# Performance work log

Measured on AMD Instinct MI355X. Metric: run time of the kernel, lower is better.

## Reference

```python
import jax, jax.numpy as jnp
import numpy as np

B, N, E = 8, 1024, 512
H, D = 8, 64
F = 2048


def setup_inputs() -> dict:
    key = jax.random.key(0)
    ks = jax.random.split(key, 12)
    s = lambda *sh: 1.0 / np.sqrt(sh[-1])
    inp = {
        "input1": jax.random.normal(ks[0], (B, N, E), dtype=jnp.float32),
        # projection weights stored as [in, out] (torch weight transposed)
        "Wq": jax.random.normal(ks[1], (E, H * D), dtype=jnp.float32) * s(E, E),
        "Wk": jax.random.normal(ks[2], (E, H * D), dtype=jnp.float32) * s(E, E),
        "Wv": jax.random.normal(ks[3], (E, H * D), dtype=jnp.float32) * s(E, E),
        "Wo": jax.random.normal(ks[4], (H * D, E), dtype=jnp.float32) * s(E, E),
        "bo": jnp.zeros((E,), dtype=jnp.float32),
        "g1": jnp.ones((E,), dtype=jnp.float32),
        "b1": jnp.zeros((E,), dtype=jnp.float32),
        "W1": jax.random.normal(ks[5], (E, F), dtype=jnp.float32) * s(E, E),
        "bf1": jnp.zeros((F,), dtype=jnp.float32),
        "W2": jax.random.normal(ks[6], (F, E), dtype=jnp.float32) * s(F, F),
        "bf2": jnp.zeros((E,), dtype=jnp.float32),
        "g2": jnp.ones((E,), dtype=jnp.float32),
        "b2": jnp.zeros((E,), dtype=jnp.float32),
    }
    return inp


def _layernorm(x, g, b, eps=1e-5):
    mu = jnp.mean(x, axis=-1, keepdims=True)
    var = jnp.var(x, axis=-1, keepdims=True)
    return (x - mu) * jax.lax.rsqrt(var + eps) * g + b


def reference(input1, Wq, Wk, Wv, Wo, bo, g1, b1, W1, bf1, W2, bf2, g2, b2):
    x = input1
    # QKV projections, split heads: [B, H, N, D]
    q = (x @ Wq).reshape(B, N, H, D).transpose(0, 2, 1, 3)
    k = (x @ Wk).reshape(B, N, H, D).transpose(0, 2, 1, 3)
    v = (x @ Wv).reshape(B, N, H, D).transpose(0, 2, 1, 3)
    # scaled dot-product attention (naive, materialized scores as in source)
    score = jnp.einsum("bhnd,bhmd->bhnm", q, k) / jnp.sqrt(jnp.float32(D))
    weights = jax.nn.softmax(score, axis=-1)
    out = jnp.einsum("bhnm,bhmd->bhnd", weights, v)
    out_concat = out.transpose(0, 2, 1, 3).reshape(B, N, H * D)
    mh = out_concat @ Wo + bo
    out1 = _layernorm(x + mh, g1, b1)
    ff = jax.nn.relu(out1 @ W1 + bf1) @ W2 + bf2
    out3 = _layernorm(out1 + ff, g2, b2)
    return (out3, 0)
```

## Files before the change

kernel.cpp:

```cpp
#include <hip/hip_runtime.h>
#include <cstdint>
#include <cstddef>

typedef _Float16 h8 __attribute__((ext_vector_type(8)));
typedef _Float16 h4 __attribute__((ext_vector_type(4)));
typedef __fp16   g2 __attribute__((ext_vector_type(2)));
typedef float    f32x4 __attribute__((ext_vector_type(4)));

constexpr int B_ = 8, N_ = 1024, E_ = 512, H_ = 8, D_ = 64, F_ = 2048;
constexpr int M_ = B_ * N_;
constexpr int HD_ = H_ * D_;

#define QSCALE2 0.18033688011112042f

#define GLOAD_LDS16(gp, lp)                                                        \
    __builtin_amdgcn_global_load_lds((const __attribute__((address_space(1))) void*)(gp), \
                                     (__attribute__((address_space(3))) void*)(lp), 16, 0, 0)

__device__ __forceinline__ float exp2_raw(float x) {
#if __has_builtin(__builtin_amdgcn_exp2f)
    return __builtin_amdgcn_exp2f(x);
#else
    float r;
    asm("v_exp_f32 %0, %1\n\ts_nop 0" : "=v"(r) : "v"(x));
    return r;
#endif
}

__global__ void __launch_bounds__(256) k_pre(
    const float* __restrict__ x, _Float16* __restrict__ xh,
    const float* __restrict__ Wq, const float* __restrict__ Wk,
    const float* __restrict__ Wv, const float* __restrict__ Wo,
    const float* __restrict__ W1, const float* __restrict__ W2,
    _Float16* __restrict__ oqkv, _Float16* __restrict__ oo,
    _Float16* __restrict__ o1, _Float16* __restrict__ o2) {
    if (blockIdx.z == 12) {
        int i = (blockIdx.x * 256 + threadIdx.x) * 16;
#pragma unroll
        for (int j = 0; j < 4; ++j) {
            float4 v = *(const float4*)(x + i + j * 4);
            h4 o = {(_Float16)v.x, (_Float16)v.y, (_Float16)v.z, (_Float16)v.w};
            *(h4*)(xh + i + j * 4) = o;
        }
        return;
    }
    if (blockIdx.x >= 256) return;
    const float* in;
    _Float16* out;
    int R, C, gt = blockIdx.x;
    switch (blockIdx.z) {
        case 0: in = Wq; out = oqkv;              R = 512;  C = 512;  break;
        case 1: in = Wk; out = oqkv + 512 * 512;  R = 512;  C = 512;  break;
        case 2: in = Wv; out = oqkv + 1024 * 512; R = 512;  C = 512;  break;
        case 3: in = Wo; out = oo;                R = 512;  C = 512;  break;
        default:
            if (blockIdx.z < 8) { in = W1; out = o1; R = 512;  C = 2048; gt += (blockIdx.z - 4) * 256; }
            else                { in = W2; out = o2; R = 2048; C = 512;  gt += (blockIdx.z - 8) * 256; }
    }
    const int ctiles = C >> 5;
    const int ty = gt / ctiles, tx = gt - ty * ctiles;
    const int r0 = ty * 32, c0 = tx * 32;
    __shared__ float lt[32][33];
    const int rr = threadIdx.x >> 3, cq = threadIdx.x & 7;
    float4 v = *(const float4*)&in[(size_t)(r0 + rr) * C + c0 + cq * 4];
    lt[rr][cq * 4 + 0] = v.x; lt[rr][cq * 4 + 1] = v.y;
    lt[rr][cq * 4 + 2] = v.z; lt[rr][cq * 4 + 3] = v.w;
    __syncthreads();
    h4 o = {(_Float16)lt[cq * 4 + 0][rr], (_Float16)lt[cq * 4 + 1][rr],
            (_Float16)lt[cq * 4 + 2][rr], (_Float16)lt[cq * 4 + 3][rr]};
    *(h4*)&out[(size_t)(c0 + rr) * R + r0 + cq * 4] = o;
}

template <int EPI>
__global__ void __launch_bounds__(256) k_gemm(
    const _Float16* __restrict__ A, const _Float16* __restrict__ Bt,
    int Mg, int Ng, int Kg,
    const float* __restrict__ bias,
    _Float16* __restrict__ outh,
    _Float16* __restrict__ qp, _Float16* __restrict__ kp, _Float16* __restrict__ vtp) {
    constexpr int BN = 128;
    constexpr int WN = BN / 2;
    constexpr int NI = WN / 16;
    constexpr int NT = 8;
    __shared__ alignas(16) _Float16 lA[3][64 * 64];
    __shared__ alignas(16) _Float16 lB[3][BN * 64];

    const int tid = threadIdx.x;
    const int lane = tid & 63;
    const int wid = tid >> 6;
    const int wr = wid >> 1, wc = wid & 1;
    const int r16 = lane & 15, hseg = lane >> 4;

    const int bid = blockIdx.x;
    const int xcd = bid & 7;
    const int rem = bid >> 3;
    const int tx = rem >> 4, tyl = rem & 15;
    const int m0 = (xcd * 16 + tyl) * 64;
    const int n0 = tx * BN;

    auto STAGE = [&](int buf, int k0) {
#pragma unroll
        for (int i = 0; i < 2; ++i) {
            const int slot = i * 256 + tid, row = slot >> 3;
            const int cs = (slot & 7) ^ (row & 7);
            GLOAD_LDS16(A + (size_t)(m0 + row) * Kg + k0 + cs * 8, &lA[buf][slot * 8]);
        }
#pragma unroll
        for (int i = 0; i < BN / 32; ++i) {
            const int slot = i * 256 + tid, row = slot >> 3;
            const int cs = (slot & 7) ^ (row & 7);
            GLOAD_LDS16(Bt + (size_t)(n0 + row) * Kg + k0 + cs * 8, &lB[buf][slot * 8]);
        }
    };

    f32x4 acc[2][NI] = {};

    auto COMPUTE = [&](const int buf) __attribute__((always_inline)) {
#pragma unroll
        for (int kk = 0; kk < 2; ++kk) {
            h8 af[2], bf[NI];
#pragma unroll
            for (int mi = 0; mi < 2; ++mi) {
                const int row = wr * 32 + mi * 16 + r16;
                af[mi] = *(const h8*)&lA[buf][row * 64 + (((kk * 4 + hseg) ^ (row & 7)) * 8)];
            }
#pragma unroll
            for (int ni = 0; ni < NI; ++ni) {
                const int row = wc * WN + ni * 16 + r16;
                bf[ni] = *(const h8*)&lB[buf][row * 64 + (((kk * 4 + hseg) ^ (row & 7)) * 8)];
            }
#pragma unroll
            for (int mi = 0; mi < 2; ++mi)
#pragma unroll
                for (int ni = 0; ni < NI; ++ni)
                    acc[mi][ni] =
                        __builtin_amdgcn_mfma_f32_16x16x32_f16(af[mi], bf[ni], acc[mi][ni], 0, 0, 0);
        }
    };

    STAGE(0, 0);
    STAGE(1, 64);
#pragma unroll
    for (int t = 0; t < NT; ++t) {
        if (t < NT - 1) asm volatile("s_waitcnt vmcnt(6)" ::: "memory");
        else            asm volatile("s_waitcnt vmcnt(0)" ::: "memory");
        __builtin_amdgcn_s_barrier();
        if (t + 2 < NT) STAGE((t + 2) % 3, (t + 2) * 64);
        COMPUTE(t % 3);
    }

    if constexpr (EPI == 0) {
        if (n0 >= 1024) {
            __syncthreads();
            _Float16* lC = &lA[0][0];
#pragma unroll
            for (int mi = 0; mi < 2; ++mi) {
                const int r0 = wr * 32 + mi * 16 + hseg * 4;
                const int s = r0 >> 3, ro = r0 & 7;
#pragma unroll
                for (int ni = 0; ni < NI; ++ni) {
                    const int c = wc * WN + ni * 16 + r16;
                    h4 pv = {(_Float16)acc[mi][ni][0], (_Float16)acc[mi][ni][1],
                             (_Float16)acc[mi][ni][2], (_Float16)acc[mi][ni][3]};
                    *(h4*)&lC[c * 64 + ((s ^ (c & 7)) << 3) + ro] = pv;
                }
            }
            __syncthreads();
            const int c = tid >> 1, half = tid & 1;
            const int b = m0 >> 10, nn0 = m0 & 1023;
            _Float16* gdst =
                vtp + ((size_t)(b * 512 + (n0 - 1024) + c)) * 1024 + nn0 + half * 32;
#pragma unroll
            for (int j = 0; j < 4; ++j) {
                const int s = half * 4 + j;
                h8 v = *(const h8*)&lC[c * 64 + ((s ^ (c & 7)) << 3)];
                *(h8*)&gdst[j * 8] = v;
            }
        } else {
#pragma unroll
            for (int mi = 0; mi < 2; ++mi)
#pragma unroll
                for (int ni = 0; ni < NI; ++ni)
#pragma unroll
                    for (int r = 0; r < 4; ++r) {
                        int row = m0 + wr * 32 + mi * 16 + hseg * 4 + r;
                        int col = n0 + wc * WN + ni * 16 + r16;
                        float v = acc[mi][ni][r];
                        int cc = col & 511;
                        int h = cc >> 6, d = cc & 63;
                        int b = row >> 10, nn = row & 1023;
                        if (col < 512)
                            qp[((b * 8 + h) * 1024 + nn) * 64 + d] = (_Float16)(v * QSCALE2);
                        else
                            kp[((b * 8 + h) * 1024 + nn) * 64 + d] = (_Float16)v;
                    }
        }
    } else {
#pragma unroll
        for (int mi = 0; mi < 2; ++mi)
#pragma unroll
            for (int ni = 0; ni < NI; ++ni)
#pragma unroll
                for (int r = 0; r < 4; ++r) {
                    int row = m0 + wr * 32 + mi * 16 + hseg * 4 + r;
                    int col = n0 + wc * WN + ni * 16 + r16;
                    float v = acc[mi][ni][r] + bias[col];
                    v = v > 0.f ? v : 0.f;
                    outh[(size_t)row * Ng + col] = (_Float16)v;
                }
    }
}

template <int NT>
__global__ void __launch_bounds__(512) k_gemm64(
    const _Float16* __restrict__ A, const _Float16* __restrict__ Bt,
    int Ng, int Kg,
    const float* __restrict__ bias,
    const _Float16* __restrict__ resh, _Float16* __restrict__ outh) {
    __shared__ alignas(16) _Float16 lA[3][128 * 64];
    __shared__ alignas(16) _Float16 lB[3][64 * 64];

    const int tid = threadIdx.x;
    const int lane = tid & 63;
    const int wid = tid >> 6;
    const int wr = wid >> 1;
    const int wc = wid & 1;
    const int r16 = lane & 15, hseg = lane >> 4;

    const int bid = blockIdx.x;
    const int xcd = bid & 7;
    const int rem = bid >> 3;
    const int tx = rem >> 3, tyl = rem & 7;
    const int m0 = (xcd * 8 + tyl) * 128;
    const int n0 = tx * 64;

    auto STAGE = [&](int buf, int k0) {
#pragma unroll
        for (int i = 0; i < 2; ++i) {
            const int slot = i * 512 + tid, row = slot >> 3;
            const int cs = (slot & 7) ^ (row & 7);
            GLOAD_LDS16(A + (size_t)(m0 + row) * Kg + k0 + cs * 8, &lA[buf][slot * 8]);
        }
        {
            const int slot = tid, row = slot >> 3;
            const int cs = (slot & 7) ^ (row & 7);
            GLOAD_LDS16(Bt + (size_t)(n0 + row) * Kg + k0 + cs * 8, &lB[buf][slot * 8]);
        }
    };

    f32x4 acc[2][2] = {};

    auto COMPUTE = [&](const int buf) __attribute__((always_inline)) {
#pragma unroll
        for (int kk = 0; kk < 2; ++kk) {
            h8 af[2], bf[2];
#pragma unroll
            for (int mi = 0; mi < 2; ++mi) {
                const int row = wr * 32 + mi * 16 + r16;
                af[mi] = *(const h8*)&lA[buf][row * 64 + (((kk * 4 + hseg) ^ (row & 7)) * 8)];
            }
#pragma unroll
            for (int ni = 0; ni < 2; ++ni) {
                const int row = wc * 32 + ni * 16 + r16;
                bf[ni] = *(const h8*)&lB[buf][row * 64 + (((kk * 4 + hseg) ^ (row & 7)) * 8)];
            }
#pragma unroll
            for (int mi = 0; mi < 2; ++mi)
#pragma unroll
                for (int ni = 0; ni < 2; ++ni)
                    acc[mi][ni] =
                        __builtin_amdgcn_mfma_f32_16x16x32_f16(af[mi], bf[ni], acc[mi][ni], 0, 0, 0);
        }
    };

    STAGE(0, 0);
    STAGE(1, 64);
#pragma unroll
    for (int t = 0; t < NT; ++t) {
        if (t < NT - 1) asm volatile("s_waitcnt vmcnt(3)" ::: "memory");
        else            asm volatile("s_waitcnt vmcnt(0)" ::: "memory");
        __builtin_amdgcn_s_barrier();
        if (t + 2 < NT) STAGE((t + 2) % 3, (t + 2) * 64);
        COMPUTE(t % 3);
    }

#pragma unroll
    for (int mi = 0; mi < 2; ++mi)
#pragma unroll
        for (int ni = 0; ni < 2; ++ni)
#pragma unroll
            for (int r = 0; r < 4; ++r) {
                int row = m0 + wr * 32 + mi * 16 + hseg * 4 + r;
                int col = n0 + wc * 32 + ni * 16 + r16;
                float v = acc[mi][ni][r] + bias[col] + (float)resh[(size_t)row * Ng + col];
                outh[(size_t)row * Ng + col] = (_Float16)v;
            }
}

__global__ void __launch_bounds__(512) k_attn(const _Float16* __restrict__ q,
                                              const _Float16* __restrict__ k,
                                              const _Float16* __restrict__ vt,
                                              _Float16* __restrict__ attn) {
    __shared__ alignas(16) _Float16 lK[2][64 * 64];
    __shared__ alignas(16) _Float16 lV[2][64 * 64];
    __shared__ alignas(16) _Float16 lP[8][16 * 64];

    const int tid = threadIdx.x, lane = tid & 63, w = tid >> 6;
    const int bid = blockIdx.x;
    const int xcd = bid & 7, rem = bid >> 3;
    const int bh = xcd * 8 + (rem & 7);
    const int q0 = (rem >> 3) * 128;
    const int r16 = lane & 15, hseg = lane >> 4;
    const size_t base = (size_t)bh * N_ * D_;

    h8 qf0 = *(const h8*)&q[base + (size_t)(q0 + w * 16 + r16) * 64 + hseg * 8];
    h8 qf1 = *(const h8*)&q[base + (size_t)(q0 + w * 16 + r16) * 64 + 32 + hseg * 8];

    const int srow = tid >> 3;
    const int scsrc = (tid & 7) ^ (srow & 7);

    auto STAGE = [&](int buf, int kt) {
        GLOAD_LDS16(k + base + kt * 4096 + srow * 64 + scsrc * 8, &lK[buf][tid * 8]);
        GLOAD_LDS16(vt + base + (size_t)srow * N_ + kt * 64 + scsrc * 8, &lV[buf][tid * 8]);
    };

    float mrun = -1e30f, lrun = 0.f;
    f32x4 oacc[4] = {};

    const char* lKb = (const char*)&lK[0][0];
    const char* lVb = (const char*)&lV[0][0];
    char* lPb = (char*)&lP[0][0] + w * 2048;
    const int swz = r16 & 7;
    const int kb0 = r16 * 128 + ((hseg ^ swz) * 16);
    const int kb1 = r16 * 128 + (((4 + hseg) ^ swz) * 16);
    const int pswz = swz * 8;
    const int prd0 = r16 * 128 + (((hseg * 8) ^ pswz) * 2);
    const int prd1 = r16 * 128 + (((32 + hseg * 8) ^ pswz) * 2);
    const int pwr0 = r16 * 128 + (((0 + hseg * 4) ^ pswz) * 2);
    const int pwr1 = r16 * 128 + (((16 + hseg * 4) ^ pswz) * 2);
    const int pwr2 = r16 * 128 + (((32 + hseg * 4) ^ pswz) * 2);
    const int pwr3 = r16 * 128 + (((48 + hseg * 4) ^ pswz) * 2);

    auto TILE = [&](const int cur, const int kt) __attribute__((always_inline)) {
        if (kt + 1 < N_ / 64) STAGE(cur ^ 1, kt + 1);
        const int cOff = cur * 8192;

        float sv[4][4];
        __builtin_amdgcn_s_setprio(1);
#pragma unroll
        for (int t4 = 0; t4 < 4; ++t4) {
            f32x4 a = {};
            h8 kf0 = *(const h8*)(lKb + cOff + t4 * 2048 + kb0);
            a = __builtin_amdgcn_mfma_f32_16x16x32_f16(kf0, qf0, a, 0, 0, 0);
            h8 kf1 = *(const h8*)(lKb + cOff + t4 * 2048 + kb1);
            a = __builtin_amdgcn_mfma_f32_16x16x32_f16(kf1, qf1, a, 0, 0, 0);
#pragma unroll
            for (int r = 0; r < 4; ++r) sv[t4][r] = a[r];
        }
        __builtin_amdgcn_s_setprio(0);

        float m0a = fmaxf(fmaxf(sv[0][0], sv[0][1]), fmaxf(sv[0][2], sv[0][3]));
        float m1a = fmaxf(fmaxf(sv[1][0], sv[1][1]), fmaxf(sv[1][2], sv[1][3]));
        float m2a = fmaxf(fmaxf(sv[2][0], sv[2][1]), fmaxf(sv[2][2], sv[2][3]));
        float m3a = fmaxf(fmaxf(sv[3][0], sv[3][1]), fmaxf(sv[3][2], sv[3][3]));
        float mx = fmaxf(fmaxf(m0a, m1a), fmaxf(m2a, m3a));

        if (__any(mx > mrun + 8.f)) {
            mx = fmaxf(mx, __shfl_xor(mx, 16));
            mx = fmaxf(mx, __shfl_xor(mx, 32));
            float mnew = fmaxf(mrun, mx);
            float sc = exp2_raw(mrun - mnew);
            mrun = mnew;
            lrun *= sc;
#pragma unroll
            for (int r = 0; r < 4; ++r) {
                float scq = __shfl(sc, hseg * 4 + r);
#pragma unroll
                for (int nf = 0; nf < 4; ++nf) oacc[nf][r] *= scq;
            }
        }

        float p[4][4];
        float rsum = 0.f;
#pragma unroll
        for (int t4 = 0; t4 < 4; ++t4)
#pragma unroll
            for (int r = 0; r < 4; ++r) {
                p[t4][r] = exp2_raw(sv[t4][r] - mrun);
                rsum += p[t4][r];
            }
        lrun += rsum;

#pragma unroll
        for (int t4 = 0; t4 < 4; ++t4) {
            g2 a0 = __builtin_amdgcn_cvt_pkrtz(p[t4][0], p[t4][1]);
            g2 a1 = __builtin_amdgcn_cvt_pkrtz(p[t4][2], p[t4][3]);
            h4 pv = {(_Float16)a0[0], (_Float16)a0[1], (_Float16)a1[0], (_Float16)a1[1]};
            char* dst = lPb + (t4 == 0 ? pwr0 : t4 == 1 ? pwr1 : t4 == 2 ? pwr2 : pwr3);
            *(h4*)dst = pv;
        }
        asm volatile("s_waitcnt lgkmcnt(0)" ::: "memory");

        h8 pa0 = *(const h8*)(lPb + prd0);
        h8 pa1 = *(const h8*)(lPb + prd1);
        __builtin_amdgcn_s_setprio(1);
#pragma unroll
        for (int nf = 0; nf < 4; ++nf) {
            h8 vb0 = *(const h8*)(lVb + cOff + nf * 2048 + kb0);
            oacc[nf] = __builtin_amdgcn_mfma_f32_16x16x32_f16(pa0, vb0, oacc[nf], 0, 0, 0);
            h8 vb1 = *(const h8*)(lVb + cOff + nf * 2048 + kb1);
            oacc[nf] = __builtin_amdgcn_mfma_f32_16x16x32_f16(pa1, vb1, oacc[nf], 0, 0, 0);
        }
        __builtin_amdgcn_s_setprio(0);
        __syncthreads();
    };

    STAGE(0, 0);
    __syncthreads();

    for (int kt = 0; kt < N_ / 64; kt += 2) {
        TILE(0, kt);
        TILE(1, kt + 1);
    }

    lrun += __shfl_xor(lrun, 16);
    lrun += __shfl_xor(lrun, 32);

    float rlin = 1.f / lrun;
    int b = bh >> 3, h = bh & 7;
#pragma unroll
    for (int r = 0; r < 4; ++r) {
        float inv = __shfl(rlin, hseg * 4 + r);
        int row = b * 1024 + q0 + w * 16 + hseg * 4 + r;
#pragma unroll
        for (int nf = 0; nf < 4; ++nf) {
            int col = h * 64 + nf * 16 + r16;
            attn[(size_t)row * 512 + col] = (_Float16)(oacc[nf][r] * inv);
        }
    }
}

template <int OUTF32>
__global__ void __launch_bounds__(256) k_ln(const _Float16* __restrict__ x,
                                            const float* __restrict__ g,
                                            const float* __restrict__ b,
                                            float* __restrict__ outf,
                                            _Float16* __restrict__ outh,
                                            float* __restrict__ tail) {
    int row = blockIdx.x * 4 + (threadIdx.x >> 6);
    int lane = threadIdx.x & 63;
    h8 v = *(const h8*)(x + (size_t)row * 512 + lane * 8);
    float f[8];
    float s = 0.f, sq = 0.f;
#pragma unroll
    for (int j = 0; j < 8; ++j) {
        f[j] = (float)v[j];
        s += f[j];
        sq += f[j] * f[j];
    }
#pragma unroll
    for (int msk = 1; msk < 64; msk <<= 1) {
        s += __shfl_xor(s, msk);
        sq += __shfl_xor(sq, msk);
    }
    float mu = s * (1.f / 512.f);
    float var = sq * (1.f / 512.f) - mu * mu;
    float rstd = rsqrtf(var + 1e-5f);
    float4 ga = *(const float4*)(g + lane * 8);
    float4 gb = *(const float4*)(g + lane * 8 + 4);
    float4 ba = *(const float4*)(b + lane * 8);
    float4 bb = *(const float4*)(b + lane * 8 + 4);
    float o[8];
    o[0] = (f[0] - mu) * rstd * ga.x + ba.x;
    o[1] = (f[1] - mu) * rstd * ga.y + ba.y;
    o[2] = (f[2] - mu) * rstd * ga.z + ba.z;
    o[3] = (f[3] - mu) * rstd * ga.w + ba.w;
    o[4] = (f[4] - mu) * rstd * gb.x + bb.x;
    o[5] = (f[5] - mu) * rstd * gb.y + bb.y;
    o[6] = (f[6] - mu) * rstd * gb.z + bb.z;
    o[7] = (f[7] - mu) * rstd * gb.w + bb.w;
    if constexpr (OUTF32) {
        float* orow = outf + (size_t)row * 512 + lane * 8;
        *(float4*)(orow) = make_float4(o[0], o[1], o[2], o[3]);
        *(float4*)(orow + 4) = make_float4(o[4], o[5], o[6], o[7]);
        if (tail && blockIdx.x == 0 && threadIdx.x == 0) tail[0] = 0.f;
    } else {
        h8 oh = {(_Float16)o[0], (_Float16)o[1], (_Float16)o[2], (_Float16)o[3],
                 (_Float16)o[4], (_Float16)o[5], (_Float16)o[6], (_Float16)o[7]};
        *(h8*)(outh + (size_t)row * 512 + lane * 8) = oh;
    }
}

extern "C" void kernel_launch(void* const* d_in, const int* in_sizes, int n_in,
                              void* d_out, int out_size, void* d_ws, size_t ws_size,
                              hipStream_t stream) {
    const float* x   = (const float*)d_in[0];
    const float* Wq  = (const float*)d_in[1];
    const float* Wk  = (const float*)d_in[2];
    const float* Wv  = (const float*)d_in[3];
    const float* Wo  = (const float*)d_in[4];
    const float* bo  = (const float*)d_in[5];
    const float* g1  = (const float*)d_in[6];
    const float* b1  = (const float*)d_in[7];
    const float* W1  = (const float*)d_in[8];
    const float* bf1 = (const float*)d_in[9];
    const float* W2  = (const float*)d_in[10];
    const float* bf2 = (const float*)d_in[11];
    const float* g2  = (const float*)d_in[12];
    const float* b2  = (const float*)d_in[13];
    float* out = (float*)d_out;

    char* ws = (char*)d_ws;
    _Float16* xh    = (_Float16*)(ws + 0);
    _Float16* wqkvT = (_Float16*)(ws + 8388608);
    _Float16* woT   = (_Float16*)(ws + 9961472);
    _Float16* w1T   = (_Float16*)(ws + 10485760);
    _Float16* w2T   = (_Float16*)(ws + 12582912);
    _Float16* qb    = (_Float16*)(ws + 14680064);
    _Float16* kb    = (_Float16*)(ws + 23068672);
    _Float16* vtb   = (_Float16*)(ws + 31457280);
    _Float16* attnb = (_Float16*)(ws + 39845888);
    _Float16* h1h   = (_Float16*)(ws + 48234496);
    _Float16* out1h = xh;
    _Float16* ff    = qb;

    k_pre<<<dim3(1024, 1, 13), 256, 0, stream>>>(x, xh, Wq, Wk, Wv, Wo, W1, W2,
                                                 wqkvT, woT, w1T, w2T);

    k_gemm<0><<<dim3(1536), 256, 0, stream>>>(
        xh, wqkvT, M_, 1536, 512, nullptr, nullptr, qb, kb, vtb);

    k_attn<<<dim3(512), 512, 0, stream>>>(qb, kb, vtb, attnb);

    k_gemm64<8><<<dim3(512), 512, 0, stream>>>(attnb, woT, 512, 512, bo, xh, h1h);

    k_ln<0><<<dim3(M_ / 4), 256, 0, stream>>>(h1h, g1, b1, nullptr, out1h, nullptr);

    k_gemm<2><<<dim3(2048), 256, 0, stream>>>(
        out1h, w1T, M_, 2048, 512, bf1, ff, nullptr, nullptr, nullptr);

    k_gemm64<32><<<dim3(512), 512, 0, stream>>>(ff, w2T, 512, 2048, bf2, out1h, h1h);

    k_ln<1><<<dim3(M_ / 4), 256, 0, stream>>>(h1h, g2, b2, out, nullptr, out + (size_t)M_ * E_);
}
```

Measured before the change: 139.2 us.

## Process two 16-row query tiles per wave in attention, halving block threads

The attention kernel now launches 256 threads (4 waves) per block instead of 512, and each wave handles 32 query rows as two 16-row groups with separate online-softmax state. Each K and V fragment read from LDS is reused for both groups, halving LDS traffic per FLOP and giving more independent MFMAs to interleave. Staging is split into two loads per thread to cover the same tiles. The cost is higher register pressure per wave and fewer waves per block, so fewer waves are available to hide latency.

```diff
diff --git a/kernel.cpp b/kernel.cpp
--- a/kernel.cpp
+++ b/kernel.cpp
@@ -297,13 +297,13 @@
             }
 }
 
-__global__ void __launch_bounds__(512) k_attn(const _Float16* __restrict__ q,
+__global__ void __launch_bounds__(256) k_attn(const _Float16* __restrict__ q,
                                               const _Float16* __restrict__ k,
                                               const _Float16* __restrict__ vt,
                                               _Float16* __restrict__ attn) {
     __shared__ alignas(16) _Float16 lK[2][64 * 64];
     __shared__ alignas(16) _Float16 lV[2][64 * 64];
-    __shared__ alignas(16) _Float16 lP[8][16 * 64];
+    __shared__ alignas(16) _Float16 lP[4][2][16 * 64];
 
     const int tid = threadIdx.x, lane = tid & 63, w = tid >> 6;
     const int bid = blockIdx.x;
@@ -313,23 +313,38 @@
     const int r16 = lane & 15, hseg = lane >> 4;
     const size_t base = (size_t)bh * N_ * D_;
 
-    h8 qf0 = *(const h8*)&q[base + (size_t)(q0 + w * 16 + r16) * 64 + hseg * 8];
-    h8 qf1 = *(const h8*)&q[base + (size_t)(q0 + w * 16 + r16) * 64 + 32 + hseg * 8];
-
-    const int srow = tid >> 3;
-    const int scsrc = (tid & 7) ^ (srow & 7);
+    const size_t qrowA = base + (size_t)(q0 + w * 32 + r16) * 64;
+    h8 qa0 = *(const h8*)&q[qrowA + hseg * 8];
+    h8 qa1 = *(const h8*)&q[qrowA + 32 + hseg * 8];
+    h8 qb0 = *(const h8*)&q[qrowA + 16 * 64 + hseg * 8];
+    h8 qb1 = *(const h8*)&q[qrowA + 16 * 64 + 32 + hseg * 8];
+
+    int srow[2], scsrc[2];
+#pragma unroll
+    for (int i = 0; i < 2; ++i) {
+        int slot = i * 256 + tid;
+        srow[i] = slot >> 3;
+        scsrc[i] = (slot & 7) ^ (srow[i] & 7);
+    }
 
     auto STAGE = [&](int buf, int kt) {
-        GLOAD_LDS16(k + base + kt * 4096 + srow * 64 + scsrc * 8, &lK[buf][tid * 8]);
-        GLOAD_LDS16(vt + base + (size_t)srow * N_ + kt * 64 + scsrc * 8, &lV[buf][tid * 8]);
+#pragma unroll
+        for (int i = 0; i < 2; ++i)
+            GLOAD_LDS16(k + base + kt * 4096 + srow[i] * 64 + scsrc[i] * 8,
+                        &lK[buf][(i * 256 + tid) * 8]);
+#pragma unroll
+        for (int i = 0; i < 2; ++i)
+            GLOAD_LDS16(vt + base + (size_t)srow[i] * N_ + kt * 64 + scsrc[i] * 8,
+                        &lV[buf][(i * 256 + tid) * 8]);
     };
 
-    float mrun = -1e30f, lrun = 0.f;
-    f32x4 oacc[4] = {};
+    float mA = -1e30f, lA_ = 0.f, mB = -1e30f, lB_ = 0.f;
+    f32x4 oA[4] = {}, oB[4] = {};
 
     const char* lKb = (const char*)&lK[0][0];
     const char* lVb = (const char*)&lV[0][0];
-    char* lPb = (char*)&lP[0][0] + w * 2048;
+    char* lPa = (char*)&lP[0][0][0] + w * 4096;
+    char* lPb2 = lPa + 2048;
     const int swz = r16 & 7;
     const int kb0 = r16 * 128 + ((hseg ^ swz) * 16);
     const int kb1 = r16 * 128 + (((4 + hseg) ^ swz) * 16);
@@ -345,71 +360,110 @@
         if (kt + 1 < N_ / 64) STAGE(cur ^ 1, kt + 1);
         const int cOff = cur * 8192;
 
-        float sv[4][4];
+        float svA[4][4], svB[4][4];
         __builtin_amdgcn_s_setprio(1);
 #pragma unroll
         for (int t4 = 0; t4 < 4; ++t4) {
+            h8 kf0 = *(const h8*)(lKb + cOff + t4 * 2048 + kb0);
+            h8 kf1 = *(const h8*)(lKb + cOff + t4 * 2048 + kb1);
             f32x4 a = {};
-            h8 kf0 = *(const h8*)(lKb + cOff + t4 * 2048 + kb0);
-            a = __builtin_amdgcn_mfma_f32_16x16x32_f16(kf0, qf0, a, 0, 0, 0);
-            h8 kf1 = *(const h8*)(lKb + cOff + t4 * 2048 + kb1);
-            a = __builtin_amdgcn_mfma_f32_16x16x32_f16(kf1, qf1, a, 0, 0, 0);
-#pragma unroll
-            for (int r = 0; r < 4; ++r) sv[t4][r] = a[r];
+            a = __builtin_amdgcn_mfma_f32_16x16x32_f16(kf0, qa0, a, 0, 0, 0);
+            a = __builtin_amdgcn_mfma_f32_16x16x32_f16(kf1, qa1, a, 0, 0, 0);
+            f32x4 b = {};
+            b = __builtin_amdgcn_mfma_f32_16x16x32_f16(kf0, qb0, b, 0, 0, 0);
+            b = __builtin_amdgcn_mfma_f32_16x16x32_f16(kf1, qb1, b, 0, 0, 0);
+#pragma unroll
+            for (int r = 0; r < 4; ++r) { svA[t4][r] = a[r]; svB[t4][r] = b[r]; }
         }
         __builtin_amdgcn_s_setprio(0);
 
-        float m0a = fmaxf(fmaxf(sv[0][0], sv[0][1]), fmaxf(sv[0][2], sv[0][3]));
-        float m1a = fmaxf(fmaxf(sv[1][0], sv[1][1]), fmaxf(sv[1][2], sv[1][3]));
-        float m2a = fmaxf(fmaxf(sv[2][0], sv[2][1]), fmaxf(sv[2][2], sv[2][3]));
-        float m3a = fmaxf(fmaxf(sv[3][0], sv[3][1]), fmaxf(sv[3][2], sv[3][3]));
-        float mx = fmaxf(fmaxf(m0a, m1a), fmaxf(m2a, m3a));
-
-        if (__any(mx > mrun + 8.f)) {
-            mx = fmaxf(mx, __shfl_xor(mx, 16));
-            mx = fmaxf(mx, __shfl_xor(mx, 32));
-            float mnew = fmaxf(mrun, mx);
-            float sc = exp2_raw(mrun - mnew);
-            mrun = mnew;
-            lrun *= sc;
-#pragma unroll
-            for (int r = 0; r < 4; ++r) {
-                float scq = __shfl(sc, hseg * 4 + r);
-#pragma unroll
-                for (int nf = 0; nf < 4; ++nf) oacc[nf][r] *= scq;
-            }
-        }
-
-        float p[4][4];
-        float rsum = 0.f;
-#pragma unroll
-        for (int t4 = 0; t4 < 4; ++t4)
-#pragma unroll
-            for (int r = 0; r < 4; ++r) {
-                p[t4][r] = exp2_raw(sv[t4][r] - mrun);
-                rsum += p[t4][r];
-            }
-        lrun += rsum;
-
-#pragma unroll
-        for (int t4 = 0; t4 < 4; ++t4) {
-            g2 a0 = __builtin_amdgcn_cvt_pkrtz(p[t4][0], p[t4][1]);
-            g2 a1 = __builtin_amdgcn_cvt_pkrtz(p[t4][2], p[t4][3]);
-            h4 pv = {(_Float16)a0[0], (_Float16)a0[1], (_Float16)a1[0], (_Float16)a1[1]};
-            char* dst = lPb + (t4 == 0 ? pwr0 : t4 == 1 ? pwr1 : t4 == 2 ? pwr2 : pwr3);
-            *(h4*)dst = pv;
+        {
+            float m0a = fmaxf(fmaxf(svA[0][0], svA[0][1]), fmaxf(svA[0][2], svA[0][3]));
+            float m1a = fmaxf(fmaxf(svA[1][0], svA[1][1]), fmaxf(svA[1][2], svA[1][3]));
+            float m2a = fmaxf(fmaxf(svA[2][0], svA[2][1]), fmaxf(svA[2][2], svA[2][3]));
+            float m3a = fmaxf(fmaxf(svA[3][0], svA[3][1]), fmaxf(svA[3][2], svA[3][3]));
+            float mx = fmaxf(fmaxf(m0a, m1a), fmaxf(m2a, m3a));
+            if (__any(mx > mA + 8.f)) {
+                mx = fmaxf(mx, __shfl_xor(mx, 16));
+                mx = fmaxf(mx, __shfl_xor(mx, 32));
+                float mnew = fmaxf(mA, mx);
+                float sc = exp2_raw(mA - mnew);
+                mA = mnew;
+                lA_ *= sc;
+#pragma unroll
+                for (int r = 0; r < 4; ++r) {
+                    float scq = __shfl(sc, hseg * 4 + r);
+#pragma unroll
+                    for (int nf = 0; nf < 4; ++nf) oA[nf][r] *= scq;
+                }
+            }
+            float rsum = 0.f;
+#pragma unroll
+            for (int t4 = 0; t4 < 4; ++t4) {
+                float p0 = exp2_raw(svA[t4][0] - mA);
+                float p1 = exp2_raw(svA[t4][1] - mA);
+                float p2 = exp2_raw(svA[t4][2] - mA);
+                float p3 = exp2_raw(svA[t4][3] - mA);
+                rsum += p0 + p1 + p2 + p3;
+                g2 a0 = __builtin_amdgcn_cvt_pkrtz(p0, p1);
+                g2 a1 = __builtin_amdgcn_cvt_pkrtz(p2, p3);
+                h4 pv = {(_Float16)a0[0], (_Float16)a0[1], (_Float16)a1[0], (_Float16)a1[1]};
+                char* dst = lPa + (t4 == 0 ? pwr0 : t4 == 1 ? pwr1 : t4 == 2 ? pwr2 : pwr3);
+                *(h4*)dst = pv;
+            }
+            lA_ += rsum;
+        }
+        {
+            float m0a = fmaxf(fmaxf(svB[0][0], svB[0][1]), fmaxf(svB[0][2], svB[0][3]));
+            float m1a = fmaxf(fmaxf(svB[1][0], svB[1][1]), fmaxf(svB[1][2], svB[1][3]));
+            float m2a = fmaxf(fmaxf(svB[2][0], svB[2][1]), fmaxf(svB[2][2], svB[2][3]));
+            float m3a = fmaxf(fmaxf(svB[3][0], svB[3][1]), fmaxf(svB[3][2], svB[3][3]));
+            float mx = fmaxf(fmaxf(m0a, m1a), fmaxf(m2a, m3a));
+            if (__any(mx > mB + 8.f)) {
+                mx = fmaxf(mx, __shfl_xor(mx, 16));
+                mx = fmaxf(mx, __shfl_xor(mx, 32));
+                float mnew = fmaxf(mB, mx);
+                float sc = exp2_raw(mB - mnew);
+                mB = mnew;
+                lB_ *= sc;
+#pragma unroll
+                for (int r = 0; r < 4; ++r) {
+                    float scq = __shfl(sc, hseg * 4 + r);
+#pragma unroll
+                    for (int nf = 0; nf < 4; ++nf) oB[nf][r] *= scq;
+                }
+            }
+            float rsum = 0.f;
+#pragma unroll
+            for (int t4 = 0; t4 < 4; ++t4) {
+                float p0 = exp2_raw(svB[t4][0] - mB);
+                float p1 = exp2_raw(svB[t4][1] - mB);
+                float p2 = exp2_raw(svB[t4][2] - mB);
+                float p3 = exp2_raw(svB[t4][3] - mB);
+                rsum += p0 + p1 + p2 + p3;
+                g2 a0 = __builtin_amdgcn_cvt_pkrtz(p0, p1);
+                g2 a1 = __builtin_amdgcn_cvt_pkrtz(p2, p3);
+                h4 pv = {(_Float16)a0[0], (_Float16)a0[1], (_Float16)a1[0], (_Float16)a1[1]};
+                char* dst = lPb2 + (t4 == 0 ? pwr0 : t4 == 1 ? pwr1 : t4 == 2 ? pwr2 : pwr3);
+                *(h4*)dst = pv;
+            }
+            lB_ += rsum;
         }
         asm volatile("s_waitcnt lgkmcnt(0)" ::: "memory");
 
-        h8 pa0 = *(const h8*)(lPb + prd0);
-        h8 pa1 = *(const h8*)(lPb + prd1);
+        h8 paA0 = *(const h8*)(lPa + prd0);
+        h8 paA1 = *(const h8*)(lPa + prd1);
+        h8 paB0 = *(const h8*)(lPb2 + prd0);
+        h8 paB1 = *(const h8*)(lPb2 + prd1);
         __builtin_amdgcn_s_setprio(1);
 #pragma unroll
         for (int nf = 0; nf < 4; ++nf) {
             h8 vb0 = *(const h8*)(lVb + cOff + nf * 2048 + kb0);
-            oacc[nf] = __builtin_amdgcn_mfma_f32_16x16x32_f16(pa0, vb0, oacc[nf], 0, 0, 0);
             h8 vb1 = *(const h8*)(lVb + cOff + nf * 2048 + kb1);
-            oacc[nf] = __builtin_amdgcn_mfma_f32_16x16x32_f16(pa1, vb1, oacc[nf], 0, 0, 0);
+            oA[nf] = __builtin_amdgcn_mfma_f32_16x16x32_f16(paA0, vb0, oA[nf], 0, 0, 0);
+            oA[nf] = __builtin_amdgcn_mfma_f32_16x16x32_f16(paA1, vb1, oA[nf], 0, 0, 0);
+            oB[nf] = __builtin_amdgcn_mfma_f32_16x16x32_f16(paB0, vb0, oB[nf], 0, 0, 0);
+            oB[nf] = __builtin_amdgcn_mfma_f32_16x16x32_f16(paB1, vb1, oB[nf], 0, 0, 0);
         }
         __builtin_amdgcn_s_setprio(0);
         __syncthreads();
@@ -423,19 +477,23 @@
         TILE(1, kt + 1);
     }
 
-    lrun += __shfl_xor(lrun, 16);
-    lrun += __shfl_xor(lrun, 32);
-
-    float rlin = 1.f / lrun;
+    lA_ += __shfl_xor(lA_, 16);
+    lA_ += __shfl_xor(lA_, 32);
+    lB_ += __shfl_xor(lB_, 16);
+    lB_ += __shfl_xor(lB_, 32);
+
+    float rlA = 1.f / lA_, rlB = 1.f / lB_;
     int b = bh >> 3, h = bh & 7;
 #pragma unroll
     for (int r = 0; r < 4; ++r) {
-        float inv = __shfl(rlin, hseg * 4 + r);
-        int row = b * 1024 + q0 + w * 16 + hseg * 4 + r;
+        float invA = __shfl(rlA, hseg * 4 + r);
+        float invB = __shfl(rlB, hseg * 4 + r);
+        int rowA = b * 1024 + q0 + w * 32 + hseg * 4 + r;
 #pragma unroll
         for (int nf = 0; nf < 4; ++nf) {
             int col = h * 64 + nf * 16 + r16;
-            attn[(size_t)row * 512 + col] = (_Float16)(oacc[nf][r] * inv);
+            attn[(size_t)rowA * 512 + col] = (_Float16)(oA[nf][r] * invA);
+            attn[(size_t)(rowA + 16) * 512 + col] = (_Float16)(oB[nf][r] * invB);
         }
     }
 }
@@ -530,7 +588,7 @@
     k_gemm<0><<<dim3(1536), 256, 0, stream>>>(
         xh, wqkvT, M_, 1536, 512, nullptr, nullptr, qb, kb, vtb);
 
-    k_attn<<<dim3(512), 512, 0, stream>>>(qb, kb, vtb, attnb);
+    k_attn<<<dim3(512), 256, 0, stream>>>(qb, kb, vtb, attnb);
 
     k_gemm64<8><<<dim3(512), 512, 0, stream>>>(attnb, woT, 512, 512, bo, xh, h1h);
 
```

After: 141.6 us. No clear change (+1.7%).
